# Performance work log

Measured on AMD Instinct MI355X. Metric: run time of the kernel, lower is better.

Reference implementation:

```python
import jax, jax.numpy as jnp
import numpy as np

NHLOG2PI = -0.5 * np.log(2.0 * np.pi)


def _log_bessel_i(nu, x):
    # log I_nu(x) via the uniform asymptotic expansion (A&S 9.7.7), accurate for large nu.
    # Replaces the original mpmath besseli loop with a device-friendly closed form.
    z = x / nu
    sq = jnp.sqrt(1.0 + z * z)
    eta = sq + jnp.log(z) - jnp.log1p(sq)
    t = 1.0 / sq
    u1 = (3.0 * t - 5.0 * t ** 3) / 24.0  # first correction term
    return nu * eta - 0.5 * jnp.log(2.0 * jnp.pi * nu) - 0.25 * jnp.log1p(z * z) + jnp.log1p(u1 / nu)


def _log_vmf_partition(d, kappa):
    # log C_d(kappa) = d*(-0.5 log 2pi) + s*log(kappa) - log I_s(kappa), s = d/2 - 1
    s = 0.5 * d - 1.0
    return d * NHLOG2PI + s * jnp.log(kappa) - _log_bessel_i(s, kappa)


def reference(id_samples, kappa_weight, prototypes, targets, project_dim):
    eps_n = 1e-12  # torch F.normalize eps
    eps_c = 1e-8   # torch cosine_similarity eps
    # --- sequential normalized EMA scatter-update of prototypes (faithful to per-sample loop) ---
    norm_samples = id_samples / jnp.maximum(
        jnp.linalg.norm(id_samples, axis=-1, keepdims=True), eps_n)

    def step(protos, inp):
        s_n, t = inp
        new = 0.05 * s_n + 0.95 * protos[t]
        new = new / jnp.maximum(jnp.linalg.norm(new), eps_n)
        return protos.at[t].set(new), None

    protos, _ = jax.lax.scan(step, prototypes, (norm_samples, targets))
    protos = jax.lax.stop_gradient(protos)  # original uses .data.detach()

    # --- cosine similarity [N, C] without materializing the repeated tensors ---
    x_n = id_samples / jnp.maximum(jnp.linalg.norm(id_samples, axis=-1, keepdims=True), eps_c)
    p_n = protos / jnp.maximum(jnp.linalg.norm(protos, axis=-1, keepdims=True), eps_c)
    cos = x_n @ p_n.T  # [N, C]

    kap = jax.nn.relu(kappa_weight)  # [C]
    logits = cos * kap[None, :]
    weight_before_exp = jnp.exp(_log_vmf_partition(float(project_dim), kap))[None, :]  # [1, C]

    # --- weighted vMF NLL ---
    num = weight_before_exp * jnp.exp(logits)
    pred = num / num.sum(-1, keepdims=True)
    p_t = jnp.take_along_axis(pred, targets[:, None], axis=1)[:, 0]
    return -jnp.mean(jnp.log(p_t + 1e-6))


def setup_inputs() -> dict:
    key = jax.random.key(0)
    k1, k2, k3 = jax.random.split(key, 3)
    N, C, D = 16384, 2048, 32
    return {
        "id_samples": jax.random.normal(k1, (N, D), dtype=jnp.float32),
        "kappa_weight": jax.random.uniform(k2, (C,), dtype=jnp.float32),
        "prototypes": jnp.zeros((C, D), dtype=jnp.float32),
        "targets": jax.random.randint(k3, (N,), 0, C),
        "project_dim": D,
    }
```

## Files before the change

kernel.cpp:

```cpp
#include <hip/hip_runtime.h>
#include <hip/hip_bf16.h>
#include <math.h>

#define D 32
#define NS2 16
#define CAP 64

typedef __attribute__((ext_vector_type(8))) short short8v;
typedef __attribute__((ext_vector_type(4))) float float4v;

static __device__ __forceinline__ unsigned short f2bf(float f) {
    union { __hip_bfloat16 h; unsigned short u; } cv;
    cv.h = __float2bfloat16(f);
    return cv.u;
}
static __device__ __forceinline__ float bf2f(unsigned short u) {
    union { float f; unsigned int i; } c;
    c.i = ((unsigned int)u) << 16;
    return c.f;
}

__global__ void k_normalize(const float* __restrict__ x, const int* __restrict__ tgt,
                            unsigned short* __restrict__ xnb,
                            int* __restrict__ cnt, int* __restrict__ list2d, int N) {
    int g = blockIdx.x * blockDim.x + threadIdx.x;
    int i = g >> 3, q = g & 7;
    if (i >= N) return;
    float4 v = ((const float4*)(x + (size_t)i * D))[q];
    float ss = v.x*v.x + v.y*v.y + v.z*v.z + v.w*v.w;
    ss += __shfl_xor(ss, 1); ss += __shfl_xor(ss, 2); ss += __shfl_xor(ss, 4);
    float nrm = fmaxf(sqrtf(ss), 1e-8f);
    ushort4 ob;
    ob.x = f2bf(v.x / nrm); ob.y = f2bf(v.y / nrm);
    ob.z = f2bf(v.z / nrm); ob.w = f2bf(v.w / nrm);
    ((ushort4*)(xnb + (size_t)i * D))[q] = ob;
    if (q == 0) {
        int t = tgt[i];
        int pos = atomicAdd(&cnt[t], 1);
        if (pos < CAP) list2d[t * CAP + pos] = i;
    }
}

__global__ void k_proto(const unsigned short* __restrict__ xnb, const int* __restrict__ tgt,
                        const int* __restrict__ list2d, const int* __restrict__ cnt,
                        const float* __restrict__ p_in, const float* __restrict__ kw,
                        unsigned short* __restrict__ qb, float* __restrict__ w,
                        int N, int C, float dval) {
    int wave = (blockIdx.x * blockDim.x + threadIdx.x) >> 6;
    int lane = threadIdx.x & 63;
    if (wave >= C) return;
    int c = wave, e = lane & 31;
    float p = p_in[(size_t)c * D + e];
    int count = cnt[c];

    if (count <= CAP) {
        int idx = (lane < count) ? list2d[c * CAP + lane] : 0x7fffffff;
        for (int it = 0; it < count; ++it) {
            int mn = idx;
            mn = min(mn, __shfl_xor(mn, 32)); mn = min(mn, __shfl_xor(mn, 16));
            mn = min(mn, __shfl_xor(mn, 8));  mn = min(mn, __shfl_xor(mn, 4));
            mn = min(mn, __shfl_xor(mn, 2));  mn = min(mn, __shfl_xor(mn, 1));
            float s = bf2f(xnb[(size_t)mn * D + e]);
            p = fmaf(0.05f, s, 0.95f * p);
            float pp = p * p;
            pp += __shfl_xor(pp, 16); pp += __shfl_xor(pp, 8); pp += __shfl_xor(pp, 4);
            pp += __shfl_xor(pp, 2);  pp += __shfl_xor(pp, 1);
            p = p / fmaxf(sqrtf(pp), 1e-12f);
            if (idx == mn) idx = 0x7fffffff;
        }
    } else {
        for (int ii = 0; ii < N; ii += 64) {
            unsigned long long m = __ballot(tgt[ii + lane] == c);
            while (m) {
                int j = __ffsll(m) - 1;
                m &= (m - 1);
                float s = bf2f(xnb[(size_t)(ii + j) * D + e]);
                p = fmaf(0.05f, s, 0.95f * p);
                float pp = p * p;
                pp += __shfl_xor(pp, 16); pp += __shfl_xor(pp, 8); pp += __shfl_xor(pp, 4);
                pp += __shfl_xor(pp, 2);  pp += __shfl_xor(pp, 1);
                p = p / fmaxf(sqrtf(pp), 1e-12f);
            }
        }
    }

    float pp = p * p;
    pp += __shfl_xor(pp, 16); pp += __shfl_xor(pp, 8); pp += __shfl_xor(pp, 4);
    pp += __shfl_xor(pp, 2);  pp += __shfl_xor(pp, 1);
    float pn = p / fmaxf(sqrtf(pp), 1e-8f);
    float kap = fmaxf(kw[c], 0.0f);
    if (lane < D) qb[(size_t)c * D + e] = f2bf(kap * pn);
    if (lane == 0) {
        float nu = 0.5f * dval - 1.0f;
        float z  = kap / nu, z2 = z * z;
        float sq = sqrtf(1.0f + z2);
        float t  = 1.0f / sq;
        float u1 = (3.0f * t - 5.0f * t * t * t) * (1.0f / 24.0f);
        float lw = dval * (-0.918938533204672742f)
                 + nu * (logf(nu) + log1pf(sq) - sq)
                 + 0.5f * logf(6.2831853071795864f * nu)
                 + 0.25f * log1pf(z2)
                 - log1pf(u1 / nu);
        w[c] = __expf(lw);
    }
}

__global__ void __launch_bounds__(256, 8)
k_slice(const unsigned short* __restrict__ xnb, const unsigned short* __restrict__ qb,
        const float* __restrict__ w, float* __restrict__ Sp, int N, int C) {
    int gw = (blockIdx.x * blockDim.x + threadIdx.x) >> 6;
    int lane = threadIdx.x & 63;
    int sl = gw >> 9;
    int sw = gw & 511;
    int s0 = sw * 32;
    int m = lane & 15, kg = lane >> 4, k0 = kg * 8;

    short8v a0 = *(const short8v*)(xnb + (size_t)(s0 + m) * D + k0);
    short8v a1 = *(const short8v*)(xnb + (size_t)(s0 + 16 + m) * D + k0);

    float4v z = {0.f, 0.f, 0.f, 0.f};
    float4v sa0 = z, sa1 = z;
    int ctbase = sl * 8;
#pragma unroll
    for (int j = 0; j < 8; ++j) {
        int c0 = (ctbase + j) * 16;
        short8v b = *(const short8v*)(qb + (size_t)(c0 + m) * D + k0);
        float wl = w[c0 + m];
        float4v acc0 = __builtin_amdgcn_mfma_f32_16x16x32_bf16(a0, b, z, 0, 0, 0);
        float4v acc1 = __builtin_amdgcn_mfma_f32_16x16x32_bf16(a1, b, z, 0, 0, 0);
#pragma unroll
        for (int r = 0; r < 4; ++r) {
            sa0[r] = fmaf(wl, __expf(acc0[r]), sa0[r]);
            sa1[r] = fmaf(wl, __expf(acc1[r]), sa1[r]);
        }
    }
#pragma unroll
    for (int off = 1; off < 16; off <<= 1) {
#pragma unroll
        for (int r = 0; r < 4; ++r) {
            sa0[r] += __shfl_xor(sa0[r], off);
            sa1[r] += __shfl_xor(sa1[r], off);
        }
    }
    if (m == 0) {
#pragma unroll
        for (int r = 0; r < 4; ++r) {
            int sA = s0 + kg * 4 + r;
            Sp[(size_t)sA * NS2 + sl] = sa0[r];
            Sp[(size_t)(sA + 16) * NS2 + sl] = sa1[r];
        }
    }
}

__global__ void k_nll(const unsigned short* __restrict__ xnb, const unsigned short* __restrict__ qb,
                      const int* __restrict__ tgt, const float* __restrict__ w,
                      const float* __restrict__ Sp, float* __restrict__ part,
                      int* __restrict__ done, float* __restrict__ out, int N, int nblk) {
    int i = blockIdx.x * blockDim.x + threadIdx.x;
    float val = 0.0f;
    if (i < N) {
        float S = 0.f;
        const float4* sp = (const float4*)(Sp + (size_t)i * NS2);
#pragma unroll
        for (int j = 0; j < NS2 / 4; ++j) { float4 v = sp[j]; S += (v.x + v.y) + (v.z + v.w); }
        int t = tgt[i];
        float d = 0.f;
        const ushort4* xa = (const ushort4*)(xnb + (size_t)i * D);
        const ushort4* qa = (const ushort4*)(qb + (size_t)t * D);
#pragma unroll
        for (int j = 0; j < D / 4; ++j) {
            ushort4 xv = xa[j], qv = qa[j];
            d = fmaf(bf2f(xv.x), bf2f(qv.x), d);
            d = fmaf(bf2f(xv.y), bf2f(qv.y), d);
            d = fmaf(bf2f(xv.z), bf2f(qv.z), d);
            d = fmaf(bf2f(xv.w), bf2f(qv.w), d);
        }
        float num = w[t] * __expf(d);
        val = logf(num / S + 1e-6f);
    }
    __shared__ float red[4];
    __shared__ int lastflag;
    val += __shfl_xor(val, 32); val += __shfl_xor(val, 16); val += __shfl_xor(val, 8);
    val += __shfl_xor(val, 4);  val += __shfl_xor(val, 2);  val += __shfl_xor(val, 1);
    if ((threadIdx.x & 63) == 0) red[threadIdx.x >> 6] = val;
    __syncthreads();
    if (threadIdx.x == 0) {
        float bp = (red[0] + red[1]) + (red[2] + red[3]);
        atomicExch((unsigned int*)&part[blockIdx.x], __float_as_uint(bp));
        __threadfence();
        int old = atomicAdd(done, 1);
        lastflag = (old == nblk - 1) ? 1 : 0;
    }
    __syncthreads();
    if (lastflag && threadIdx.x < 64) {
        __threadfence();
        unsigned int u = atomicAdd((unsigned int*)&part[threadIdx.x], 0u);
        float v = (threadIdx.x < nblk) ? __uint_as_float(u) : 0.f;
        v += __shfl_xor(v, 32); v += __shfl_xor(v, 16); v += __shfl_xor(v, 8);
        v += __shfl_xor(v, 4);  v += __shfl_xor(v, 2);  v += __shfl_xor(v, 1);
        if (threadIdx.x == 0) out[0] = -v / (float)N;
    }
}

extern "C" void kernel_launch(void* const* d_in, const int* in_sizes, int n_in,
                              void* d_out, int out_size, void* d_ws, size_t ws_size,
                              hipStream_t stream) {
    const float* x    = (const float*)d_in[0];
    const float* kw   = (const float*)d_in[1];
    const float* p_in = (const float*)d_in[2];
    const int*   tgt  = (const int*)d_in[3];
    int C = in_sizes[1];
    int N = in_sizes[3];
    float dval = (float)(in_sizes[2] / C);

    unsigned short* xnb = (unsigned short*)d_ws;
    unsigned short* qb  = xnb + (size_t)N * D;
    float* w    = (float*)(qb + (size_t)C * D);
    float* Sp   = w + C;
    float* part = Sp + (size_t)N * NS2;
    int* cnt    = (int*)(part + 64);
    int* done   = cnt + C;
    int* list2d = done + 1;
    (void)n_in; (void)out_size; (void)ws_size;

    int nblk = N / 256;

    hipMemsetAsync(cnt, 0, (size_t)(C + 1) * sizeof(int), stream);
    k_normalize<<<(N * 8 + 255) / 256, 256, 0, stream>>>(x, tgt, xnb, cnt, list2d, N);
    k_proto<<<(C * 64 + 255) / 256, 256, 0, stream>>>(xnb, tgt, list2d, cnt, p_in, kw, qb, w, N, C, dval);
    k_slice<<<((N / 32) * NS2) / 4, 256, 0, stream>>>(xnb, qb, w, Sp, N, C);
    k_nll<<<nblk, 256, 0, stream>>>(xnb, qb, tgt, w, Sp, part, done, (float*)d_out, N, nblk);
}
```

Before: 44.54 us.

## Fuse all stages into one persistent kernel with software grid barriers

```diff
diff --git a/kernel.cpp b/kernel.cpp
--- a/kernel.cpp
+++ b/kernel.cpp
@@ -3,8 +3,9 @@
 #include <math.h>
 
 #define D 32
-#define NS2 16
 #define CAP 64
+#define PRE 24
+#define BT 256
 
 typedef __attribute__((ext_vector_type(8))) short short8v;
 typedef __attribute__((ext_vector_type(4))) float float4v;
@@ -20,185 +21,216 @@
     return c.f;
 }
 
-__global__ void k_normalize(const float* __restrict__ x, const int* __restrict__ tgt,
-                            unsigned short* __restrict__ xnb,
-                            int* __restrict__ cnt, int* __restrict__ list2d, int N) {
-    int g = blockIdx.x * blockDim.x + threadIdx.x;
-    int i = g >> 3, q = g & 7;
-    if (i >= N) return;
-    float4 v = ((const float4*)(x + (size_t)i * D))[q];
-    float ss = v.x*v.x + v.y*v.y + v.z*v.z + v.w*v.w;
-    ss += __shfl_xor(ss, 1); ss += __shfl_xor(ss, 2); ss += __shfl_xor(ss, 4);
-    float nrm = fmaxf(sqrtf(ss), 1e-8f);
-    ushort4 ob;
-    ob.x = f2bf(v.x / nrm); ob.y = f2bf(v.y / nrm);
-    ob.z = f2bf(v.z / nrm); ob.w = f2bf(v.w / nrm);
-    ((ushort4*)(xnb + (size_t)i * D))[q] = ob;
-    if (q == 0) {
-        int t = tgt[i];
-        int pos = atomicAdd(&cnt[t], 1);
-        if (pos < CAP) list2d[t * CAP + pos] = i;
-    }
-}
-
-__global__ void k_proto(const unsigned short* __restrict__ xnb, const int* __restrict__ tgt,
-                        const int* __restrict__ list2d, const int* __restrict__ cnt,
-                        const float* __restrict__ p_in, const float* __restrict__ kw,
-                        unsigned short* __restrict__ qb, float* __restrict__ w,
-                        int N, int C, float dval) {
-    int wave = (blockIdx.x * blockDim.x + threadIdx.x) >> 6;
-    int lane = threadIdx.x & 63;
-    if (wave >= C) return;
-    int c = wave, e = lane & 31;
-    float p = p_in[(size_t)c * D + e];
-    int count = cnt[c];
-
-    if (count <= CAP) {
-        int idx = (lane < count) ? list2d[c * CAP + lane] : 0x7fffffff;
-        for (int it = 0; it < count; ++it) {
-            int mn = idx;
-            mn = min(mn, __shfl_xor(mn, 32)); mn = min(mn, __shfl_xor(mn, 16));
-            mn = min(mn, __shfl_xor(mn, 8));  mn = min(mn, __shfl_xor(mn, 4));
-            mn = min(mn, __shfl_xor(mn, 2));  mn = min(mn, __shfl_xor(mn, 1));
-            float s = bf2f(xnb[(size_t)mn * D + e]);
-            p = fmaf(0.05f, s, 0.95f * p);
+static __device__ __forceinline__ void gbar(int* ctr, int nblk) {
+    __syncthreads();
+    if (threadIdx.x == 0) {
+        __threadfence();
+        atomicAdd(ctr, 1);
+        while (atomicAdd(ctr, 0) < nblk) __builtin_amdgcn_s_sleep(2);
+        __threadfence();
+    }
+    __syncthreads();
+}
+
+__global__ void __launch_bounds__(BT, 2)
+k_mega(const float* __restrict__ x, const float* __restrict__ kw,
+       const float* __restrict__ p_in, const int* __restrict__ tgt,
+       unsigned short* __restrict__ xnb, unsigned short* __restrict__ qb,
+       float* __restrict__ w, int* __restrict__ cnt, int* __restrict__ list2d,
+       int* __restrict__ bar, float* __restrict__ part, int* __restrict__ done,
+       float* __restrict__ out, int N, int C, float dval, int nblk)
+{
+    int tid = threadIdx.x, b = blockIdx.x;
+    int lane = tid & 63, wv = tid >> 6;
+
+    {
+        int g = b * BT + tid;
+        int i = g >> 3, q = g & 7;
+        if (i < N) {
+            float4 v = ((const float4*)(x + (size_t)i * D))[q];
+            float ss = v.x*v.x + v.y*v.y + v.z*v.z + v.w*v.w;
+            ss += __shfl_xor(ss, 1); ss += __shfl_xor(ss, 2); ss += __shfl_xor(ss, 4);
+            float nrm = fmaxf(sqrtf(ss), 1e-8f);
+            ushort4 ob;
+            ob.x = f2bf(v.x / nrm); ob.y = f2bf(v.y / nrm);
+            ob.z = f2bf(v.z / nrm); ob.w = f2bf(v.w / nrm);
+            ((ushort4*)(xnb + (size_t)i * D))[q] = ob;
+            if (q == 0) {
+                int t = tgt[i];
+                int pos = atomicAdd(&cnt[t], 1);
+                if (pos < CAP) list2d[t * CAP + pos] = i;
+            }
+        }
+    }
+    gbar(&bar[0], nblk);
+
+    {
+        int c = b * (BT / 64) + wv;
+        if (c < C) {
+            int e = lane & 31;
+            float p = p_in[(size_t)c * D + e];
+            int count = cnt[c];
+            if (count <= PRE) {
+                int idx = (lane < count) ? list2d[c * CAP + lane] : 0x7fffffff;
+                int rank = 0;
+                for (int j = 0; j < count; ++j) {
+                    int v = __shfl(idx, j);
+                    rank += (v < idx) ? 1 : 0;
+                }
+                int sorted = 0;
+                for (int j = 0; j < count; ++j) {
+                    int v = __shfl(idx, j); int r = __shfl(rank, j);
+                    if (r == lane) sorted = v;
+                }
+                float vals[PRE];
+#pragma unroll
+                for (int it = 0; it < PRE; ++it)
+                    if (it < count) {
+                        int si = __shfl(sorted, it);
+                        vals[it] = bf2f(xnb[(size_t)si * D + e]);
+                    }
+#pragma unroll
+                for (int it = 0; it < PRE; ++it)
+                    if (it < count) {
+                        p = fmaf(0.05f, vals[it], 0.95f * p);
+                        float pp = p * p;
+                        pp += __shfl_xor(pp, 16); pp += __shfl_xor(pp, 8); pp += __shfl_xor(pp, 4);
+                        pp += __shfl_xor(pp, 2);  pp += __shfl_xor(pp, 1);
+                        p = p / fmaxf(sqrtf(pp), 1e-12f);
+                    }
+            } else if (count <= CAP) {
+                int idx = (lane < count) ? list2d[c * CAP + lane] : 0x7fffffff;
+                for (int it = 0; it < count; ++it) {
+                    int mn = idx;
+                    mn = min(mn, __shfl_xor(mn, 32)); mn = min(mn, __shfl_xor(mn, 16));
+                    mn = min(mn, __shfl_xor(mn, 8));  mn = min(mn, __shfl_xor(mn, 4));
+                    mn = min(mn, __shfl_xor(mn, 2));  mn = min(mn, __shfl_xor(mn, 1));
+                    float s = bf2f(xnb[(size_t)mn * D + e]);
+                    p = fmaf(0.05f, s, 0.95f * p);
+                    float pp = p * p;
+                    pp += __shfl_xor(pp, 16); pp += __shfl_xor(pp, 8); pp += __shfl_xor(pp, 4);
+                    pp += __shfl_xor(pp, 2);  pp += __shfl_xor(pp, 1);
+                    p = p / fmaxf(sqrtf(pp), 1e-12f);
+                    if (idx == mn) idx = 0x7fffffff;
+                }
+            } else {
+                for (int ii = 0; ii < N; ii += 64) {
+                    unsigned long long m = __ballot(tgt[ii + lane] == c);
+                    while (m) {
+                        int j = __ffsll(m) - 1;
+                        m &= (m - 1);
+                        float s = bf2f(xnb[(size_t)(ii + j) * D + e]);
+                        p = fmaf(0.05f, s, 0.95f * p);
+                        float pp = p * p;
+                        pp += __shfl_xor(pp, 16); pp += __shfl_xor(pp, 8); pp += __shfl_xor(pp, 4);
+                        pp += __shfl_xor(pp, 2);  pp += __shfl_xor(pp, 1);
+                        p = p / fmaxf(sqrtf(pp), 1e-12f);
+                    }
+                }
+            }
             float pp = p * p;
             pp += __shfl_xor(pp, 16); pp += __shfl_xor(pp, 8); pp += __shfl_xor(pp, 4);
             pp += __shfl_xor(pp, 2);  pp += __shfl_xor(pp, 1);
-            p = p / fmaxf(sqrtf(pp), 1e-12f);
-            if (idx == mn) idx = 0x7fffffff;
-        }
-    } else {
-        for (int ii = 0; ii < N; ii += 64) {
-            unsigned long long m = __ballot(tgt[ii + lane] == c);
-            while (m) {
-                int j = __ffsll(m) - 1;
-                m &= (m - 1);
-                float s = bf2f(xnb[(size_t)(ii + j) * D + e]);
-                p = fmaf(0.05f, s, 0.95f * p);
-                float pp = p * p;
-                pp += __shfl_xor(pp, 16); pp += __shfl_xor(pp, 8); pp += __shfl_xor(pp, 4);
-                pp += __shfl_xor(pp, 2);  pp += __shfl_xor(pp, 1);
-                p = p / fmaxf(sqrtf(pp), 1e-12f);
-            }
-        }
-    }
-
-    float pp = p * p;
-    pp += __shfl_xor(pp, 16); pp += __shfl_xor(pp, 8); pp += __shfl_xor(pp, 4);
-    pp += __shfl_xor(pp, 2);  pp += __shfl_xor(pp, 1);
-    float pn = p / fmaxf(sqrtf(pp), 1e-8f);
-    float kap = fmaxf(kw[c], 0.0f);
-    if (lane < D) qb[(size_t)c * D + e] = f2bf(kap * pn);
-    if (lane == 0) {
-        float nu = 0.5f * dval - 1.0f;
-        float z  = kap / nu, z2 = z * z;
-        float sq = sqrtf(1.0f + z2);
-        float t  = 1.0f / sq;
-        float u1 = (3.0f * t - 5.0f * t * t * t) * (1.0f / 24.0f);
-        float lw = dval * (-0.918938533204672742f)
-                 + nu * (logf(nu) + log1pf(sq) - sq)
-                 + 0.5f * logf(6.2831853071795864f * nu)
-                 + 0.25f * log1pf(z2)
-                 - log1pf(u1 / nu);
-        w[c] = __expf(lw);
-    }
-}
-
-__global__ void __launch_bounds__(256, 8)
-k_slice(const unsigned short* __restrict__ xnb, const unsigned short* __restrict__ qb,
-        const float* __restrict__ w, float* __restrict__ Sp, int N, int C) {
-    int gw = (blockIdx.x * blockDim.x + threadIdx.x) >> 6;
-    int lane = threadIdx.x & 63;
-    int sl = gw >> 9;
-    int sw = gw & 511;
-    int s0 = sw * 32;
-    int m = lane & 15, kg = lane >> 4, k0 = kg * 8;
-
-    short8v a0 = *(const short8v*)(xnb + (size_t)(s0 + m) * D + k0);
-    short8v a1 = *(const short8v*)(xnb + (size_t)(s0 + 16 + m) * D + k0);
-
-    float4v z = {0.f, 0.f, 0.f, 0.f};
-    float4v sa0 = z, sa1 = z;
-    int ctbase = sl * 8;
-#pragma unroll
-    for (int j = 0; j < 8; ++j) {
-        int c0 = (ctbase + j) * 16;
-        short8v b = *(const short8v*)(qb + (size_t)(c0 + m) * D + k0);
-        float wl = w[c0 + m];
-        float4v acc0 = __builtin_amdgcn_mfma_f32_16x16x32_bf16(a0, b, z, 0, 0, 0);
-        float4v acc1 = __builtin_amdgcn_mfma_f32_16x16x32_bf16(a1, b, z, 0, 0, 0);
-#pragma unroll
-        for (int r = 0; r < 4; ++r) {
-            sa0[r] = fmaf(wl, __expf(acc0[r]), sa0[r]);
-            sa1[r] = fmaf(wl, __expf(acc1[r]), sa1[r]);
-        }
-    }
-#pragma unroll
-    for (int off = 1; off < 16; off <<= 1) {
-#pragma unroll
-        for (int r = 0; r < 4; ++r) {
-            sa0[r] += __shfl_xor(sa0[r], off);
-            sa1[r] += __shfl_xor(sa1[r], off);
-        }
-    }
-    if (m == 0) {
-#pragma unroll
-        for (int r = 0; r < 4; ++r) {
-            int sA = s0 + kg * 4 + r;
-            Sp[(size_t)sA * NS2 + sl] = sa0[r];
-            Sp[(size_t)(sA + 16) * NS2 + sl] = sa1[r];
-        }
-    }
-}
-
-__global__ void k_nll(const unsigned short* __restrict__ xnb, const unsigned short* __restrict__ qb,
-                      const int* __restrict__ tgt, const float* __restrict__ w,
-                      const float* __restrict__ Sp, float* __restrict__ part,
-                      int* __restrict__ done, float* __restrict__ out, int N, int nblk) {
-    int i = blockIdx.x * blockDim.x + threadIdx.x;
-    float val = 0.0f;
-    if (i < N) {
-        float S = 0.f;
-        const float4* sp = (const float4*)(Sp + (size_t)i * NS2);
-#pragma unroll
-        for (int j = 0; j < NS2 / 4; ++j) { float4 v = sp[j]; S += (v.x + v.y) + (v.z + v.w); }
-        int t = tgt[i];
-        float d = 0.f;
-        const ushort4* xa = (const ushort4*)(xnb + (size_t)i * D);
-        const ushort4* qa = (const ushort4*)(qb + (size_t)t * D);
-#pragma unroll
-        for (int j = 0; j < D / 4; ++j) {
-            ushort4 xv = xa[j], qv = qa[j];
-            d = fmaf(bf2f(xv.x), bf2f(qv.x), d);
-            d = fmaf(bf2f(xv.y), bf2f(qv.y), d);
-            d = fmaf(bf2f(xv.z), bf2f(qv.z), d);
-            d = fmaf(bf2f(xv.w), bf2f(qv.w), d);
-        }
-        float num = w[t] * __expf(d);
-        val = logf(num / S + 1e-6f);
-    }
-    __shared__ float red[4];
+            float pn = p / fmaxf(sqrtf(pp), 1e-8f);
+            float kap = fmaxf(kw[c], 0.0f);
+            if (lane < D) qb[(size_t)c * D + e] = f2bf(kap * pn);
+            if (lane == 0) {
+                float nu = 0.5f * dval - 1.0f;
+                float z  = kap / nu, z2 = z * z;
+                float sq = sqrtf(1.0f + z2);
+                float t  = 1.0f / sq;
+                float u1 = (3.0f * t - 5.0f * t * t * t) * (1.0f / 24.0f);
+                float lw = dval * (-0.918938533204672742f)
+                         + nu * (logf(nu) + log1pf(sq) - sq)
+                         + 0.5f * logf(6.2831853071795864f * nu)
+                         + 0.25f * log1pf(z2)
+                         - log1pf(u1 / nu);
+                w[c] = __expf(lw);
+            }
+        }
+    }
+    gbar(&bar[1], nblk);
+
+    __shared__ float Sl[4][32];
+    __shared__ float redv[4];
+    __shared__ float red2[4];
     __shared__ int lastflag;
-    val += __shfl_xor(val, 32); val += __shfl_xor(val, 16); val += __shfl_xor(val, 8);
-    val += __shfl_xor(val, 4);  val += __shfl_xor(val, 2);  val += __shfl_xor(val, 1);
-    if ((threadIdx.x & 63) == 0) red[threadIdx.x >> 6] = val;
-    __syncthreads();
-    if (threadIdx.x == 0) {
-        float bp = (red[0] + red[1]) + (red[2] + red[3]);
-        atomicExch((unsigned int*)&part[blockIdx.x], __float_as_uint(bp));
+    {
+        int m = lane & 15, kg = lane >> 4, k0 = kg * 8;
+        int s0 = b * 32;
+        short8v a0 = *(const short8v*)(xnb + (size_t)(s0 + m) * D + k0);
+        short8v a1 = *(const short8v*)(xnb + (size_t)(s0 + 16 + m) * D + k0);
+        float4v z = {0.f, 0.f, 0.f, 0.f};
+        float4v sa0 = z, sa1 = z;
+        int nct = C / 64;
+        for (int jt = 0; jt < nct; ++jt) {
+            int c0 = (wv * nct + jt) * 16;
+            short8v bf = *(const short8v*)(qb + (size_t)(c0 + m) * D + k0);
+            float wl = w[c0 + m];
+            float4v acc0 = __builtin_amdgcn_mfma_f32_16x16x32_bf16(a0, bf, z, 0, 0, 0);
+            float4v acc1 = __builtin_amdgcn_mfma_f32_16x16x32_bf16(a1, bf, z, 0, 0, 0);
+#pragma unroll
+            for (int r = 0; r < 4; ++r) {
+                sa0[r] = fmaf(wl, __expf(acc0[r]), sa0[r]);
+                sa1[r] = fmaf(wl, __expf(acc1[r]), sa1[r]);
+            }
+        }
+#pragma unroll
+        for (int off = 1; off < 16; off <<= 1) {
+#pragma unroll
+            for (int r = 0; r < 4; ++r) {
+                sa0[r] += __shfl_xor(sa0[r], off);
+                sa1[r] += __shfl_xor(sa1[r], off);
+            }
+        }
+        if (m == 0) {
+#pragma unroll
+            for (int r = 0; r < 4; ++r) {
+                Sl[wv][kg * 4 + r]      = sa0[r];
+                Sl[wv][16 + kg * 4 + r] = sa1[r];
+            }
+        }
+    }
+    __syncthreads();
+    {
+        int s_sub = wv * 8 + (lane >> 3);
+        int e4 = (lane & 7) * 4;
+        int si = b * 32 + s_sub;
+        int t = tgt[si];
+        ushort4 xv = *(const ushort4*)(xnb + (size_t)si * D + e4);
+        ushort4 qv = *(const ushort4*)(qb + (size_t)t * D + e4);
+        float d4 = bf2f(xv.x) * bf2f(qv.x);
+        d4 = fmaf(bf2f(xv.y), bf2f(qv.y), d4);
+        d4 = fmaf(bf2f(xv.z), bf2f(qv.z), d4);
+        d4 = fmaf(bf2f(xv.w), bf2f(qv.w), d4);
+        d4 += __shfl_xor(d4, 1); d4 += __shfl_xor(d4, 2); d4 += __shfl_xor(d4, 4);
+        float val = 0.f;
+        if ((lane & 7) == 0) {
+            float S = (Sl[0][s_sub] + Sl[1][s_sub]) + (Sl[2][s_sub] + Sl[3][s_sub]);
+            val = logf(w[t] * __expf(d4) / S + 1e-6f);
+        }
+        val += __shfl_xor(val, 8); val += __shfl_xor(val, 16); val += __shfl_xor(val, 32);
+        if (lane == 0) redv[wv] = val;
+    }
+    __syncthreads();
+    if (tid == 0) {
+        float bp = (redv[0] + redv[1]) + (redv[2] + redv[3]);
+        atomicExch((unsigned int*)&part[b], __float_as_uint(bp));
         __threadfence();
         int old = atomicAdd(done, 1);
         lastflag = (old == nblk - 1) ? 1 : 0;
     }
     __syncthreads();
-    if (lastflag && threadIdx.x < 64) {
-        __threadfence();
-        unsigned int u = atomicAdd((unsigned int*)&part[threadIdx.x], 0u);
-        float v = (threadIdx.x < nblk) ? __uint_as_float(u) : 0.f;
-        v += __shfl_xor(v, 32); v += __shfl_xor(v, 16); v += __shfl_xor(v, 8);
-        v += __shfl_xor(v, 4);  v += __shfl_xor(v, 2);  v += __shfl_xor(v, 1);
-        if (threadIdx.x == 0) out[0] = -v / (float)N;
+    if (lastflag) {
+        __threadfence();
+        float v = 0.f;
+        if (tid < nblk)      v += __uint_as_float(atomicAdd((unsigned int*)&part[tid], 0u));
+        if (tid + BT < nblk) v += __uint_as_float(atomicAdd((unsigned int*)&part[tid + BT], 0u));
+        v += __shfl_xor(v, 1); v += __shfl_xor(v, 2); v += __shfl_xor(v, 4);
+        v += __shfl_xor(v, 8); v += __shfl_xor(v, 16); v += __shfl_xor(v, 32);
+        if (lane == 0) red2[wv] = v;
+        __syncthreads();
+        if (tid == 0) out[0] = -((red2[0] + red2[1]) + (red2[2] + red2[3])) / (float)N;
     }
 }
 
@@ -212,22 +244,20 @@
     int C = in_sizes[1];
     int N = in_sizes[3];
     float dval = (float)(in_sizes[2] / C);
-
-    unsigned short* xnb = (unsigned short*)d_ws;
+    int nblk = N / 32;
+
+    int* cnt  = (int*)d_ws;
+    int* done = cnt + C;
+    int* bar  = done + 1;
+    size_t zbytes = ((size_t)(C + 16) * sizeof(int) + 63) & ~(size_t)63;
+    unsigned short* xnb = (unsigned short*)((char*)d_ws + zbytes);
     unsigned short* qb  = xnb + (size_t)N * D;
     float* w    = (float*)(qb + (size_t)C * D);
-    float* Sp   = w + C;
-    float* part = Sp + (size_t)N * NS2;
-    int* cnt    = (int*)(part + 64);
-    int* done   = cnt + C;
-    int* list2d = done + 1;
+    float* part = w + C;
+    int* list2d = (int*)(part + nblk);
     (void)n_in; (void)out_size; (void)ws_size;
 
-    int nblk = N / 256;
-
-    hipMemsetAsync(cnt, 0, (size_t)(C + 1) * sizeof(int), stream);
-    k_normalize<<<(N * 8 + 255) / 256, 256, 0, stream>>>(x, tgt, xnb, cnt, list2d, N);
-    k_proto<<<(C * 64 + 255) / 256, 256, 0, stream>>>(xnb, tgt, list2d, cnt, p_in, kw, qb, w, N, C, dval);
-    k_slice<<<((N / 32) * NS2) / 4, 256, 0, stream>>>(xnb, qb, w, Sp, N, C);
-    k_nll<<<nblk, 256, 0, stream>>>(xnb, qb, tgt, w, Sp, part, done, (float*)d_out, N, nblk);
-}
+    hipMemsetAsync(d_ws, 0, (size_t)(C + 16) * sizeof(int), stream);
+    k_mega<<<nblk, BT, 0, stream>>>(x, kw, p_in, tgt, xnb, qb, w, cnt, list2d,
+                                    bar, part, done, (float*)d_out, N, C, dval, nblk);
+}
```

Result: slower. 134.2 us (+201.3%).
